# Kernel tuning notes

Measured on AMD Instinct MI355X. Metric: run time of the kernel, lower is better.

Reference implementation:

```python
import jax, jax.numpy as jnp
import numpy as np

N = 100000   # nodes
E = 600000   # edges
D = 128      # hidden_dim
R = 8        # edge_vocab_size (num_relations)
B = 64       # graphs in batch
V = 5000     # node_vocab_size
L = 3        # num_layers


def setup_inputs() -> dict:
    key = jax.random.key(0)
    ks = jax.random.split(key, 16)
    s = 1.0 / np.sqrt(D)
    node_type = jax.random.randint(ks[0], (N,), 0, V, dtype=jnp.int32)
    edge_index = jax.random.randint(ks[1], (2, E), 0, N, dtype=jnp.int32)
    edge_type = jax.random.randint(ks[2], (E,), 0, R, dtype=jnp.int32)
    batch = jnp.sort(jax.random.randint(ks[3], (N,), 0, B, dtype=jnp.int32))
    node_emb = jax.random.normal(ks[4], (V, D), dtype=jnp.float32)
    rel_w = jax.random.normal(ks[5], (L, R, D, D), dtype=jnp.float32) * s
    root_w = jax.random.normal(ks[6], (L, D, D), dtype=jnp.float32) * s
    bias = jnp.zeros((L, D), dtype=jnp.float32)
    risk_w1 = jax.random.normal(ks[7], (D, D), dtype=jnp.float32) * s
    risk_b1 = jnp.zeros((D,), dtype=jnp.float32)
    risk_w2 = jax.random.normal(ks[8], (D, 1), dtype=jnp.float32) * s
    risk_b2 = jnp.zeros((1,), dtype=jnp.float32)
    safe_w1 = jax.random.normal(ks[9], (D, D), dtype=jnp.float32) * s
    safe_b1 = jnp.zeros((D,), dtype=jnp.float32)
    safe_w2 = jax.random.normal(ks[10], (D, 1), dtype=jnp.float32) * s
    safe_b2 = jnp.zeros((1,), dtype=jnp.float32)
    return dict(node_type=node_type, edge_index=edge_index, edge_type=edge_type,
                batch=batch, node_emb=node_emb, rel_w=rel_w, root_w=root_w,
                bias=bias, risk_w1=risk_w1, risk_b1=risk_b1, risk_w2=risk_w2,
                risk_b2=risk_b2, safe_w1=safe_w1, safe_b1=safe_b1,
                safe_w2=safe_w2, safe_b2=safe_b2)


def _rgcn_layer(x, edge_index, edge_type, Wrel, Wroot, b):
    # PyG RGCNConv: per-relation mean aggregation of source features,
    # then relation-specific linear + root transform + bias.
    src, dst = edge_index[0], edge_index[1]
    seg = dst * R + edge_type                      # combined (node, relation) id
    msgs = x[src]                                  # [E, D] gather
    sums = jax.ops.segment_sum(msgs, seg, num_segments=N * R)      # [N*R, D]
    cnt = jax.ops.segment_sum(jnp.ones((E,), x.dtype), seg, num_segments=N * R)
    mean = sums / jnp.maximum(cnt, 1.0)[:, None]
    mean = mean.reshape(N, R, D)
    out = jnp.einsum('nrd,rde->ne', mean, Wrel) + x @ Wroot + b
    return out


def _mlp_head(g, w1, b1, w2, b2):
    h = jax.nn.relu(g @ w1 + b1)
    return (h @ w2 + b2).squeeze(-1)               # dropout is identity in eval


def reference(node_type, edge_index, edge_type, batch, node_emb, rel_w, root_w,
              bias, risk_w1, risk_b1, risk_w2, risk_b2, safe_w1, safe_b1,
              safe_w2, safe_b2):
    x = node_emb[node_type]                        # [N, D]
    for l in range(L):                             # fixed small layer loop
        x = jax.nn.relu(_rgcn_layer(x, edge_index, edge_type,
                                    rel_w[l], root_w[l], bias[l]))
    # global_mean_pool over graph ids
    g_sum = jax.ops.segment_sum(x, batch, num_segments=B)          # [B, D]
    g_cnt = jax.ops.segment_sum(jnp.ones((N,), x.dtype), batch, num_segments=B)
    g = g_sum / jnp.maximum(g_cnt, 1.0)[:, None]
    risk_pred = _mlp_head(g, risk_w1, risk_b1, risk_w2, risk_b2)   # [B]
    safe_logit = _mlp_head(g, safe_w1, safe_b1, safe_w2, safe_b2)  # [B]
    return risk_pred, safe_logit
```

## Files before the change

kernel.cpp:

```cpp
#include <hip/hip_runtime.h>
#include <hip/hip_bf16.h>

#define N_NODES 100000
#define N_EDGES 600000
#define DIM     128
#define N_REL   8
#define N_GRAPH 64
#define N_LAYER 3
#define NR      (N_NODES * N_REL)
#define NB1     782

typedef __attribute__((ext_vector_type(4))) float float4v;
typedef __attribute__((ext_vector_type(2))) float float2v;
typedef unsigned long long ull;

__device__ __forceinline__ int gswz8(int row, int g) {
    return row * 16 + (g ^ (row & 15));
}

__global__ void k_hist(const int* __restrict__ ei, const int* __restrict__ et,
                       int* __restrict__ counts) {
    int e = blockIdx.x * 256 + threadIdx.x;
    if (e < N_EDGES) {
        int seg = ei[N_EDGES + e] * N_REL + et[e];
        atomicAdd(&counts[seg], 1);
    }
}

__global__ __launch_bounds__(256) void k_scan1(const int* __restrict__ cnts,
                                               int* __restrict__ part,
                                               int* __restrict__ bsum) {
    __shared__ int sh[256];
    int t = threadIdx.x;
    int base = blockIdx.x * 1024 + t * 4;
    int v0 = (base + 0 < NR) ? cnts[base + 0] : 0;
    int v1 = (base + 1 < NR) ? cnts[base + 1] : 0;
    int v2 = (base + 2 < NR) ? cnts[base + 2] : 0;
    int v3 = (base + 3 < NR) ? cnts[base + 3] : 0;
    int tot = v0 + v1 + v2 + v3;
    sh[t] = tot;
    __syncthreads();
    for (int off = 1; off < 256; off <<= 1) {
        int x = (t >= off) ? sh[t - off] : 0;
        __syncthreads();
        sh[t] += x;
        __syncthreads();
    }
    int exc = sh[t] - tot;
    if (base + 0 < NR) part[base + 0] = exc;
    if (base + 1 < NR) part[base + 1] = exc + v0;
    if (base + 2 < NR) part[base + 2] = exc + v0 + v1;
    if (base + 3 < NR) part[base + 3] = exc + v0 + v1 + v2;
    if (t == 255) bsum[blockIdx.x] = sh[t];
}

__global__ __launch_bounds__(1024) void k_scan2(int* __restrict__ bsum, int nb) {
    __shared__ int sh[1024];
    int t = threadIdx.x;
    int v = (t < nb) ? bsum[t] : 0;
    sh[t] = v;
    __syncthreads();
    for (int off = 1; off < 1024; off <<= 1) {
        int x = (t >= off) ? sh[t - off] : 0;
        __syncthreads();
        sh[t] += x;
        __syncthreads();
    }
    if (t < nb) bsum[t] = sh[t] - v;
}

__global__ void k_scan3(const int* __restrict__ part, const int* __restrict__ bsum,
                        int* __restrict__ rowptr, int* __restrict__ cursor) {
    int i = blockIdx.x * 256 + threadIdx.x;
    if (i < NR) {
        int v = part[i] + bsum[i >> 10];
        rowptr[i] = v;
        cursor[i] = v;
    }
    if (i == 0) rowptr[NR] = N_EDGES;
}

__global__ void k_scatter(const int* __restrict__ ei, const int* __restrict__ et,
                          int* __restrict__ cursor, int* __restrict__ srcs) {
    int e = blockIdx.x * 256 + threadIdx.x;
    if (e < N_EDGES) {
        int seg = ei[N_EDGES + e] * N_REL + et[e];
        int p = atomicAdd(&cursor[seg], 1);
        srcs[p] = ei[e];
    }
}

__global__ void k_gather8(const int* __restrict__ nt, const float* __restrict__ emb,
                          unsigned int* __restrict__ x8) {
    int gid = blockIdx.x * 256 + threadIdx.x;
    if (gid < N_NODES * 32) {
        int n = gid >> 5, up = gid & 31;
        const float* row = emb + (size_t)nt[n] * DIM;
        int p0 = up * 4;
        float f0 = row[((p0 + 0) & 7) * 16 + ((p0 + 0) >> 3)];
        float f1 = row[((p0 + 1) & 7) * 16 + ((p0 + 1) >> 3)];
        float f2 = row[((p0 + 2) & 7) * 16 + ((p0 + 2) >> 3)];
        float f3 = row[((p0 + 3) & 7) * 16 + ((p0 + 3) >> 3)];
        int u = __builtin_amdgcn_cvt_pk_fp8_f32(f0, f1, 0, false);
        u = __builtin_amdgcn_cvt_pk_fp8_f32(f2, f3, u, true);
        x8[gid] = (unsigned int)u;
    }
}

#define W8_TOTAL (N_LAYER * 9 * 8192)
__global__ void k_wprep9(const float* __restrict__ relw, const float* __restrict__ rootw,
                         unsigned short* __restrict__ W8) {
    int gid = blockIdx.x * 256 + threadIdx.x;
    if (gid < W8_TOTAL) {
        int l = gid / (9 * 8192);
        int rem = gid - l * 9 * 8192;
        int r = rem >> 13;
        int idx = rem & 8191;
        int n = idx >> 6, p2 = idx & 63;
        int pos0 = 2 * p2, pos1 = 2 * p2 + 1;
        int k0 = (pos0 & 7) * 16 + (pos0 >> 3);
        int k1 = (pos1 & 7) * 16 + (pos1 >> 3);
        float w0, w1;
        if (r < 8) {
            const float* base = relw + ((size_t)(l * 8 + r) * 128) * 128 + n;
            w0 = base[(size_t)k0 * 128];
            w1 = base[(size_t)k1 * 128];
        } else {
            const float* base = rootw + (size_t)l * 128 * 128 + n;
            w0 = base[(size_t)k0 * 128];
            w1 = base[(size_t)k1 * 128];
        }
        int pk = __builtin_amdgcn_cvt_pk_fp8_f32(w0, w1, 0, false);
        W8[gid] = (unsigned short)(pk & 0xffff);
    }
}

__global__ __launch_bounds__(256) void k_agg(
    const unsigned int* __restrict__ x8,
    const int* __restrict__ rowptr,
    const int* __restrict__ srcs,
    unsigned int* __restrict__ Ag8,
    int d0, int rows, int srows)
{
    const int t = threadIdx.x;
    const int wv = t >> 6, lane = t & 63;
    const int q = lane >> 4, j = lane & 15;
    const int nb0 = (blockIdx.x * 4 + wv) * 4;
    if (nb0 >= rows) return;
    const int myn = nb0 + q;
    const bool nvalid = (myn < rows);

    int pr = 0;
    {
        int idx = (d0 + nb0) * 8 + lane;
        if (idx > NR) idx = NR;
        if (lane < 33) pr = rowptr[idx];
    }
    const int P0 = __shfl(pr, 0);
    const int Dtot = __shfl(pr, 32) - P0;

    int my_src = 0;
    if (lane < Dtot) my_src = srcs[P0 + lane];

    const uint2* x2p = (const uint2*)x8;
    uint2* Agf = (uint2*)Ag8;

    for (int r = 0; r < 8; ++r) {
        int e0 = __shfl(pr, q * 8 + r);
        int e1 = __shfl(pr, q * 8 + r + 1);
        int cnt = e1 - e0;
        int m1 = max(cnt, __shfl_xor(cnt, 16));
        int maxc = max(m1, __shfl_xor(m1, 32));
        float2v A0 = {0.f, 0.f}, A1 = {0.f, 0.f}, A2 = {0.f, 0.f}, A3 = {0.f, 0.f};
        int k = 0;
        for (; k + 2 <= maxc; k += 2) {
            int ei0 = e0 + k, ei1 = e0 + k + 1;
            int r0 = ei0 - P0, r1 = ei1 - P0;
            int s0 = __shfl(my_src, r0 & 63);
            int s1 = __shfl(my_src, r1 & 63);
            if (r0 >= 64) s0 = srcs[ei0];
            if (r1 >= 64) s1 = srcs[ei1];
            bool v0 = (k < cnt), v1 = (k + 1 < cnt);
            uint2 u0, u1;
            if (v0) u0 = x2p[(size_t)s0 * 16 + j];
            if (v1) u1 = x2p[(size_t)s1 * 16 + j];
            if (v0) {
                A0 += __builtin_amdgcn_cvt_pk_f32_fp8((int)u0.x, false);
                A1 += __builtin_amdgcn_cvt_pk_f32_fp8((int)u0.x, true);
                A2 += __builtin_amdgcn_cvt_pk_f32_fp8((int)u0.y, false);
                A3 += __builtin_amdgcn_cvt_pk_f32_fp8((int)u0.y, true);
            }
            if (v1) {
                A0 += __builtin_amdgcn_cvt_pk_f32_fp8((int)u1.x, false);
                A1 += __builtin_amdgcn_cvt_pk_f32_fp8((int)u1.x, true);
                A2 += __builtin_amdgcn_cvt_pk_f32_fp8((int)u1.y, false);
                A3 += __builtin_amdgcn_cvt_pk_f32_fp8((int)u1.y, true);
            }
        }
        if (k < maxc) {
            int ei = e0 + k;
            int ridx = ei - P0;
            int s = __shfl(my_src, ridx & 63);
            if (ridx >= 64) s = srcs[ei];
            if (k < cnt) {
                uint2 u = x2p[(size_t)s * 16 + j];
                A0 += __builtin_amdgcn_cvt_pk_f32_fp8((int)u.x, false);
                A1 += __builtin_amdgcn_cvt_pk_f32_fp8((int)u.x, true);
                A2 += __builtin_amdgcn_cvt_pk_f32_fp8((int)u.y, false);
                A3 += __builtin_amdgcn_cvt_pk_f32_fp8((int)u.y, true);
            }
        }
        float inv = (cnt > 0) ? 1.0f / (float)cnt : 0.f;
        float2v iv = {inv, inv};
        A0 *= iv; A1 *= iv; A2 *= iv; A3 *= iv;
        int u0 = __builtin_amdgcn_cvt_pk_fp8_f32(A0.x, A0.y, 0, false);
        u0 = __builtin_amdgcn_cvt_pk_fp8_f32(A1.x, A1.y, u0, true);
        int u1 = __builtin_amdgcn_cvt_pk_fp8_f32(A2.x, A2.y, 0, false);
        u1 = __builtin_amdgcn_cvt_pk_fp8_f32(A3.x, A3.y, u1, true);
        if (nvalid) {
            uint2 v; v.x = (unsigned int)u0; v.y = (unsigned int)u1;
            Agf[(size_t)r * srows * 16 + (size_t)(myn >> 4) * 256 + j * 16 + (myn & 15)] = v;
        }
    }
}

#define BM2 128
__global__ __launch_bounds__(256) void k_gemm(
    const unsigned int* __restrict__ Ag8,
    const unsigned int* __restrict__ x8in,
    unsigned int* __restrict__ x8out,
    const unsigned short* __restrict__ W8,
    const float* __restrict__ bias,
    int d0, int srows)
{
    __shared__ __align__(16) ull Bls[4096];
    const int t = threadIdx.x;
    const int wv = t >> 6, lane = t & 63;
    const int quad = lane >> 4, l15 = lane & 15;
    const int m0 = d0 + blockIdx.x * BM2;

    float4v acc[2][8];
#pragma unroll
    for (int nt = 0; nt < 8; ++nt) {
        float bc = bias[nt * 16 + l15];
        acc[0][nt] = (float4v){bc, bc, bc, bc};
        acc[1][nt] = (float4v){bc, bc, bc, bc};
    }

    const size_t pstride = (size_t)srows * 16;
    const ull* Ag = (const ull*)Ag8 + ((size_t)((m0 - d0) >> 4) + 2 * wv) * 256;
    const ull* Xr = (const ull*)x8in;

    ull aC[8], aN[8], bR[8];
    {
        const ull* Wc = (const ull*)W8;
#pragma unroll
        for (int i = 0; i < 8; ++i) {
            aC[i] = Ag[(size_t)(i >> 2) * 256 + (i & 3) * 64 + lane];
            bR[i] = Wc[t + 256 * i];
        }
    }
#pragma unroll
    for (int i = 0; i < 8; ++i) {
        int idx = t + 256 * i;
        Bls[gswz8(idx >> 4, idx & 15)] = bR[i];
    }
    __syncthreads();

    for (int c = 0; c < 9; ++c) {
        const int cur = (c & 1) * 2048;
        if (c < 8) {
            if (c + 1 < 8) {
                const ull* Ac = Ag + (size_t)(c + 1) * pstride;
#pragma unroll
                for (int i = 0; i < 8; ++i)
                    aN[i] = Ac[(size_t)(i >> 2) * 256 + (i & 3) * 64 + lane];
            } else {
#pragma unroll
                for (int i = 0; i < 8; ++i) {
                    int rt = i >> 2, kk = i & 3;
                    aN[i] = Xr[(size_t)(m0 + wv * 32 + rt * 16 + l15) * 16 + kk * 4 + quad];
                }
            }
            const ull* Wc = (const ull*)(W8 + (size_t)(c + 1) * 8192);
#pragma unroll
            for (int i = 0; i < 8; ++i) bR[i] = Wc[t + 256 * i];
        }
#pragma unroll
        for (int kk = 0; kk < 4; ++kk) {
            long long a0 = (long long)aC[kk];
            long long a1 = (long long)aC[4 + kk];
            int g = kk * 4 + quad;
#pragma unroll
            for (int nt = 0; nt < 8; ++nt) {
                long long b8 = (long long)Bls[cur + (nt * 16 + l15) * 16 + (g ^ l15)];
                acc[0][nt] = __builtin_amdgcn_mfma_f32_16x16x32_fp8_fp8(a0, b8, acc[0][nt], 0, 0, 0);
                acc[1][nt] = __builtin_amdgcn_mfma_f32_16x16x32_fp8_fp8(a1, b8, acc[1][nt], 0, 0, 0);
            }
        }
        if (c < 8) {
            const int nxt = ((c + 1) & 1) * 2048;
#pragma unroll
            for (int i = 0; i < 8; ++i) {
                int idx = t + 256 * i;
                Bls[nxt + gswz8(idx >> 4, idx & 15)] = bR[i];
                aC[i] = aN[i];
            }
            __syncthreads();
        }
    }
    ull* outs = (ull*)x8out;
#pragma unroll
    for (int rt = 0; rt < 2; ++rt) {
#pragma unroll
        for (int i = 0; i < 4; ++i) {
            int row = m0 + wv * 32 + rt * 16 + quad * 4 + i;
            float v0 = acc[rt][0][i], v1 = acc[rt][1][i];
            float v2 = acc[rt][2][i], v3 = acc[rt][3][i];
            float v4 = acc[rt][4][i], v5 = acc[rt][5][i];
            float v6 = acc[rt][6][i], v7 = acc[rt][7][i];
            v0 = v0 > 0.f ? v0 : 0.f;  v1 = v1 > 0.f ? v1 : 0.f;
            v2 = v2 > 0.f ? v2 : 0.f;  v3 = v3 > 0.f ? v3 : 0.f;
            v4 = v4 > 0.f ? v4 : 0.f;  v5 = v5 > 0.f ? v5 : 0.f;
            v6 = v6 > 0.f ? v6 : 0.f;  v7 = v7 > 0.f ? v7 : 0.f;
            int lo = __builtin_amdgcn_cvt_pk_fp8_f32(v0, v1, 0, false);
            lo = __builtin_amdgcn_cvt_pk_fp8_f32(v2, v3, lo, true);
            int hi = __builtin_amdgcn_cvt_pk_fp8_f32(v4, v5, 0, false);
            hi = __builtin_amdgcn_cvt_pk_fp8_f32(v6, v7, hi, true);
            if (row < N_NODES) {
                ull w = ((ull)(unsigned int)hi << 32) | (unsigned int)lo;
                outs[(size_t)row * 16 + l15] = w;
            }
        }
    }
}

__global__ __launch_bounds__(256) void k_pool(const unsigned int* __restrict__ x8,
                                              const int* __restrict__ batch,
                                              float* __restrict__ gsum,
                                              int* __restrict__ gcnt) {
    const int wv = threadIdx.x >> 6, lane = threadIdx.x & 63;
    const int n0 = (blockIdx.x * 4 + wv) * 64;
    if (n0 >= N_NODES) return;
    int n1 = n0 + 64;
    if (n1 > N_NODES) n1 = N_NODES;
    const int nb = n1 - n0;
    const unsigned short* xs = (const unsigned short*)x8;
    int bb = batch[n0 + (lane < nb ? lane : nb - 1)];
    float2v A = {0.f, 0.f};
    int run = 0;
    int cur = __shfl(bb, 0);
    for (int base = 0; base < nb; base += 8) {
        unsigned int u[8];
        int m = nb - base;
#pragma unroll
        for (int qq = 0; qq < 8; ++qq)
            if (qq < m) u[qq] = xs[(size_t)(n0 + base + qq) * 64 + lane];
#pragma unroll
        for (int qq = 0; qq < 8; ++qq) {
            if (qq < m) {
                int b = __shfl(bb, base + qq);
                if (b != cur) {
                    atomicAdd(&gsum[cur * 128 + lane * 2], A.x);
                    atomicAdd(&gsum[cur * 128 + lane * 2 + 1], A.y);
                    if (lane == 0) atomicAdd(&gcnt[cur], run);
                    A = (float2v){0.f, 0.f};
                    run = 0;
                    cur = b;
                }
                A += __builtin_amdgcn_cvt_pk_f32_fp8((int)u[qq], false);
                ++run;
            }
        }
    }
    atomicAdd(&gsum[cur * 128 + lane * 2], A.x);
    atomicAdd(&gsum[cur * 128 + lane * 2 + 1], A.y);
    if (lane == 0) atomicAdd(&gcnt[cur], run);
}

__global__ __launch_bounds__(128) void k_heads(
    const float* __restrict__ gsum, const int* __restrict__ gcnt,
    const float* __restrict__ rw1, const float* __restrict__ rb1,
    const float* __restrict__ rw2, const float* __restrict__ rb2,
    const float* __restrict__ sw1, const float* __restrict__ sb1,
    const float* __restrict__ sw2, const float* __restrict__ sb2,
    float* __restrict__ out) {
    __shared__ float g[128];
    __shared__ float parts[2];
    int b = blockIdx.x, t = threadIdx.x;
    int c = gcnt[b];
    float invc = 1.0f / (float)(c > 0 ? c : 1);
    g[((t & 7) << 4) | (t >> 3)] = gsum[b * 128 + t] * invc;
    __syncthreads();
    float acc = rb1[t];
    for (int d = 0; d < 128; ++d) acc += g[d] * rw1[d * 128 + t];
    float h = acc > 0.f ? acc : 0.f;
    float p = h * rw2[t];
    for (int o = 32; o > 0; o >>= 1) p += __shfl_down(p, o);
    if ((t & 63) == 0) parts[t >> 6] = p;
    __syncthreads();
    if (t == 0) out[b] = parts[0] + parts[1] + rb2[0];
    __syncthreads();
    acc = sb1[t];
    for (int d = 0; d < 128; ++d) acc += g[d] * sw1[d * 128 + t];
    h = acc > 0.f ? acc : 0.f;
    p = h * sw2[t];
    for (int o = 32; o > 0; o >>= 1) p += __shfl_down(p, o);
    if ((t & 63) == 0) parts[t >> 6] = p;
    __syncthreads();
    if (t == 0) out[64 + b] = parts[0] + parts[1] + sb2[0];
}

extern "C" void kernel_launch(void* const* d_in, const int* in_sizes, int n_in,
                              void* d_out, int out_size, void* d_ws, size_t ws_size,
                              hipStream_t stream) {
    const int*   node_type  = (const int*)d_in[0];
    const int*   edge_index = (const int*)d_in[1];
    const int*   edge_type  = (const int*)d_in[2];
    const int*   batch      = (const int*)d_in[3];
    const float* node_emb   = (const float*)d_in[4];
    const float* rel_w      = (const float*)d_in[5];
    const float* root_w     = (const float*)d_in[6];
    const float* bias       = (const float*)d_in[7];
    const float* rw1        = (const float*)d_in[8];
    const float* rb1        = (const float*)d_in[9];
    const float* rw2        = (const float*)d_in[10];
    const float* rb2        = (const float*)d_in[11];
    const float* sw1        = (const float*)d_in[12];
    const float* sb1        = (const float*)d_in[13];
    const float* sw2        = (const float*)d_in[14];
    const float* sb2        = (const float*)d_in[15];
    float* out = (float*)d_out;

    char* ws = (char*)d_ws;
    size_t off = 0;
    auto alloc = [&](size_t bytes) -> void* {
        void* p = ws + off;
        off += (bytes + 255) & ~(size_t)255;
        return p;
    };
    unsigned int*   x8a    = (unsigned int*)alloc((size_t)N_NODES * 32 * 4);
    unsigned int*   x8b    = (unsigned int*)alloc((size_t)N_NODES * 32 * 4);
    int*            rowptr = (int*)alloc((size_t)(NR + 1) * 4);
    int*            srcs   = (int*)alloc((size_t)N_EDGES * 4);
    int*            bsum   = (int*)alloc(1024 * 4);
    unsigned short* W8     = (unsigned short*)alloc((size_t)W8_TOTAL * 2);
    float*          gsum   = (float*)alloc((64 * 128 + 64) * 4);
    int*            gcnt   = (int*)(gsum + 64 * 128);
    size_t off_common = off;
    int*            cursor = (int*)alloc((size_t)NR * 4);
    int*            counts = (int*)alloc((size_t)NR * 4);
    size_t off_sort = off;
    if (off_sort > ws_size) return;
    unsigned int*   Ag8    = (unsigned int*)(ws + off_common);
    size_t avail = ws_size - off_common;
    long max_rows = (avail > 32768) ? (long)((avail - 32768) / 1024) : 0;
    int srows = (int)((max_rows / 64) * 64);
    if (srows > N_NODES + 63) srows = ((N_NODES + 63) / 64) * 64;
    if (srows < 128) return;

    hipMemsetAsync(counts, 0, (size_t)NR * 4, stream);
    hipMemsetAsync(gsum, 0, (size_t)(64 * 128 + 64) * 4, stream);
    k_hist<<<(N_EDGES + 255) / 256, 256, 0, stream>>>(edge_index, edge_type, counts);
    k_scan1<<<NB1, 256, 0, stream>>>(counts, cursor, bsum);
    k_scan2<<<1, 1024, 0, stream>>>(bsum, NB1);
    k_scan3<<<(NR + 255) / 256, 256, 0, stream>>>(cursor, bsum, rowptr, cursor);
    k_scatter<<<(N_EDGES + 255) / 256, 256, 0, stream>>>(edge_index, edge_type, cursor, srcs);

    k_gather8<<<(N_NODES * 32 + 255) / 256, 256, 0, stream>>>(node_type, node_emb, x8a);
    k_wprep9<<<(W8_TOTAL + 255) / 256, 256, 0, stream>>>(rel_w, root_w, W8);

    unsigned int* xcur = x8a;
    unsigned int* xnext = x8b;
    for (int l = 0; l < N_LAYER; ++l) {
        const unsigned short* W8l = W8 + (size_t)l * 9 * 8192;
        const float* bl = bias + (size_t)l * 128;
        for (int d0 = 0; d0 < N_NODES; d0 += srows) {
            int rows = N_NODES - d0;
            if (rows > srows) rows = srows;
            int ab = (rows + 15) / 16;
            int gb = (rows + BM2 - 1) / BM2;
            k_agg<<<ab, 256, 0, stream>>>(xcur, rowptr, srcs, Ag8, d0, rows, srows);
            k_gemm<<<gb, 256, 0, stream>>>(Ag8, xcur, xnext, W8l, bl, d0, srows);
        }
        unsigned int* tmp = xcur; xcur = xnext; xnext = tmp;
    }

    k_pool<<<(N_NODES + 255) / 256, 256, 0, stream>>>(xcur, batch, gsum, gcnt);
    k_heads<<<64, 128, 0, stream>>>(gsum, gcnt, rw1, rb1, rw2, rb2,
                                    sw1, sb1, sw2, sb2, out);
}
```

Measured before the change: 421.9 us.

## Merge prep kernels and fuse mean pooling into last-layer GEMM epilogue

Combines the histogram, embedding gather, weight prep and graph-count kernels into one block-partitioned prep launch to cut launch overhead. The final layer's GEMM no longer writes fp8 node features; it accumulates ReLU outputs straight into per-graph sums, first through LDS slots and then global atomics, which removes the separate pool kernel and one fp8 round-trip. The pooled sums now stay in fp32 rather than going through fp8 quantisation, and the chunk size is rounded to 128 rows. The cost is heavy LDS and global atomic traffic in the last GEMM epilogue.

```diff
diff --git a/kernel.cpp b/kernel.cpp
--- a/kernel.cpp
+++ b/kernel.cpp
@@ -18,82 +18,29 @@
     return row * 16 + (g ^ (row & 15));
 }
 
-__global__ void k_hist(const int* __restrict__ ei, const int* __restrict__ et,
-                       int* __restrict__ counts) {
-    int e = blockIdx.x * 256 + threadIdx.x;
-    if (e < N_EDGES) {
-        int seg = ei[N_EDGES + e] * N_REL + et[e];
-        atomicAdd(&counts[seg], 1);
-    }
-}
-
-__global__ __launch_bounds__(256) void k_scan1(const int* __restrict__ cnts,
-                                               int* __restrict__ part,
-                                               int* __restrict__ bsum) {
-    __shared__ int sh[256];
-    int t = threadIdx.x;
-    int base = blockIdx.x * 1024 + t * 4;
-    int v0 = (base + 0 < NR) ? cnts[base + 0] : 0;
-    int v1 = (base + 1 < NR) ? cnts[base + 1] : 0;
-    int v2 = (base + 2 < NR) ? cnts[base + 2] : 0;
-    int v3 = (base + 3 < NR) ? cnts[base + 3] : 0;
-    int tot = v0 + v1 + v2 + v3;
-    sh[t] = tot;
-    __syncthreads();
-    for (int off = 1; off < 256; off <<= 1) {
-        int x = (t >= off) ? sh[t - off] : 0;
-        __syncthreads();
-        sh[t] += x;
-        __syncthreads();
-    }
-    int exc = sh[t] - tot;
-    if (base + 0 < NR) part[base + 0] = exc;
-    if (base + 1 < NR) part[base + 1] = exc + v0;
-    if (base + 2 < NR) part[base + 2] = exc + v0 + v1;
-    if (base + 3 < NR) part[base + 3] = exc + v0 + v1 + v2;
-    if (t == 255) bsum[blockIdx.x] = sh[t];
-}
-
-__global__ __launch_bounds__(1024) void k_scan2(int* __restrict__ bsum, int nb) {
-    __shared__ int sh[1024];
-    int t = threadIdx.x;
-    int v = (t < nb) ? bsum[t] : 0;
-    sh[t] = v;
-    __syncthreads();
-    for (int off = 1; off < 1024; off <<= 1) {
-        int x = (t >= off) ? sh[t - off] : 0;
-        __syncthreads();
-        sh[t] += x;
-        __syncthreads();
-    }
-    if (t < nb) bsum[t] = sh[t] - v;
-}
-
-__global__ void k_scan3(const int* __restrict__ part, const int* __restrict__ bsum,
-                        int* __restrict__ rowptr, int* __restrict__ cursor) {
-    int i = blockIdx.x * 256 + threadIdx.x;
-    if (i < NR) {
-        int v = part[i] + bsum[i >> 10];
-        rowptr[i] = v;
-        cursor[i] = v;
-    }
-    if (i == 0) rowptr[NR] = N_EDGES;
-}
-
-__global__ void k_scatter(const int* __restrict__ ei, const int* __restrict__ et,
-                          int* __restrict__ cursor, int* __restrict__ srcs) {
-    int e = blockIdx.x * 256 + threadIdx.x;
-    if (e < N_EDGES) {
-        int seg = ei[N_EDGES + e] * N_REL + et[e];
-        int p = atomicAdd(&cursor[seg], 1);
-        srcs[p] = ei[e];
-    }
-}
-
-__global__ void k_gather8(const int* __restrict__ nt, const float* __restrict__ emb,
-                          unsigned int* __restrict__ x8) {
-    int gid = blockIdx.x * 256 + threadIdx.x;
-    if (gid < N_NODES * 32) {
+#define W8_TOTAL (N_LAYER * 9 * 8192)
+#define PB_HIST  2344
+#define PB_GATH  12500
+#define PB_WPRE  864
+#define PB_BCNT  391
+#define PB_TOTAL (PB_HIST + PB_GATH + PB_WPRE + PB_BCNT)
+
+__global__ __launch_bounds__(256) void k_prep(
+    const int* __restrict__ ei, const int* __restrict__ et, int* __restrict__ counts,
+    const int* __restrict__ nt, const float* __restrict__ emb, unsigned int* __restrict__ x8,
+    const float* __restrict__ relw, const float* __restrict__ rootw,
+    unsigned short* __restrict__ W8,
+    const int* __restrict__ batch, int* __restrict__ gcnt)
+{
+    const int b = blockIdx.x, t = threadIdx.x;
+    if (b < PB_HIST) {
+        int e = b * 256 + t;
+        if (e < N_EDGES) {
+            int seg = ei[N_EDGES + e] * N_REL + et[e];
+            atomicAdd(&counts[seg], 1);
+        }
+    } else if (b < PB_HIST + PB_GATH) {
+        int gid = (b - PB_HIST) * 256 + t;
         int n = gid >> 5, up = gid & 31;
         const float* row = emb + (size_t)nt[n] * DIM;
         int p0 = up * 4;
@@ -104,14 +51,8 @@
         int u = __builtin_amdgcn_cvt_pk_fp8_f32(f0, f1, 0, false);
         u = __builtin_amdgcn_cvt_pk_fp8_f32(f2, f3, u, true);
         x8[gid] = (unsigned int)u;
-    }
-}
-
-#define W8_TOTAL (N_LAYER * 9 * 8192)
-__global__ void k_wprep9(const float* __restrict__ relw, const float* __restrict__ rootw,
-                         unsigned short* __restrict__ W8) {
-    int gid = blockIdx.x * 256 + threadIdx.x;
-    if (gid < W8_TOTAL) {
+    } else if (b < PB_HIST + PB_GATH + PB_WPRE) {
+        int gid = (b - PB_HIST - PB_GATH) * 256 + t;
         int l = gid / (9 * 8192);
         int rem = gid - l * 9 * 8192;
         int r = rem >> 13;
@@ -132,6 +73,72 @@
         }
         int pk = __builtin_amdgcn_cvt_pk_fp8_f32(w0, w1, 0, false);
         W8[gid] = (unsigned short)(pk & 0xffff);
+    } else {
+        int i = (b - PB_HIST - PB_GATH - PB_WPRE) * 256 + t;
+        if (i < N_NODES) atomicAdd(&gcnt[batch[i]], 1);
+    }
+}
+
+__global__ __launch_bounds__(256) void k_scan1(const int* __restrict__ cnts,
+                                               int* __restrict__ part,
+                                               int* __restrict__ bsum) {
+    __shared__ int sh[256];
+    int t = threadIdx.x;
+    int base = blockIdx.x * 1024 + t * 4;
+    int v0 = (base + 0 < NR) ? cnts[base + 0] : 0;
+    int v1 = (base + 1 < NR) ? cnts[base + 1] : 0;
+    int v2 = (base + 2 < NR) ? cnts[base + 2] : 0;
+    int v3 = (base + 3 < NR) ? cnts[base + 3] : 0;
+    int tot = v0 + v1 + v2 + v3;
+    sh[t] = tot;
+    __syncthreads();
+    for (int off = 1; off < 256; off <<= 1) {
+        int x = (t >= off) ? sh[t - off] : 0;
+        __syncthreads();
+        sh[t] += x;
+        __syncthreads();
+    }
+    int exc = sh[t] - tot;
+    if (base + 0 < NR) part[base + 0] = exc;
+    if (base + 1 < NR) part[base + 1] = exc + v0;
+    if (base + 2 < NR) part[base + 2] = exc + v0 + v1;
+    if (base + 3 < NR) part[base + 3] = exc + v0 + v1 + v2;
+    if (t == 255) bsum[blockIdx.x] = sh[t];
+}
+
+__global__ __launch_bounds__(1024) void k_scan2(int* __restrict__ bsum, int nb) {
+    __shared__ int sh[1024];
+    int t = threadIdx.x;
+    int v = (t < nb) ? bsum[t] : 0;
+    sh[t] = v;
+    __syncthreads();
+    for (int off = 1; off < 1024; off <<= 1) {
+        int x = (t >= off) ? sh[t - off] : 0;
+        __syncthreads();
+        sh[t] += x;
+        __syncthreads();
+    }
+    if (t < nb) bsum[t] = sh[t] - v;
+}
+
+__global__ void k_scan3(const int* __restrict__ part, const int* __restrict__ bsum,
+                        int* __restrict__ rowptr, int* __restrict__ cursor) {
+    int i = blockIdx.x * 256 + threadIdx.x;
+    if (i < NR) {
+        int v = part[i] + bsum[i >> 10];
+        rowptr[i] = v;
+        cursor[i] = v;
+    }
+    if (i == 0) rowptr[NR] = N_EDGES;
+}
+
+__global__ void k_scatter(const int* __restrict__ ei, const int* __restrict__ et,
+                          int* __restrict__ cursor, int* __restrict__ srcs) {
+    int e = blockIdx.x * 256 + threadIdx.x;
+    if (e < N_EDGES) {
+        int seg = ei[N_EDGES + e] * N_REL + et[e];
+        int p = atomicAdd(&cursor[seg], 1);
+        srcs[p] = ei[e];
     }
 }
 
@@ -231,7 +238,9 @@
     unsigned int* __restrict__ x8out,
     const unsigned short* __restrict__ W8,
     const float* __restrict__ bias,
-    int d0, int srows)
+    const int* __restrict__ batch,
+    float* __restrict__ gsum,
+    int d0, int srows, int last)
 {
     __shared__ __align__(16) ull Bls[4096];
     const int t = threadIdx.x;
@@ -309,73 +318,62 @@
             __syncthreads();
         }
     }
-    ull* outs = (ull*)x8out;
-#pragma unroll
-    for (int rt = 0; rt < 2; ++rt) {
-#pragma unroll
-        for (int i = 0; i < 4; ++i) {
-            int row = m0 + wv * 32 + rt * 16 + quad * 4 + i;
-            float v0 = acc[rt][0][i], v1 = acc[rt][1][i];
-            float v2 = acc[rt][2][i], v3 = acc[rt][3][i];
-            float v4 = acc[rt][4][i], v5 = acc[rt][5][i];
-            float v6 = acc[rt][6][i], v7 = acc[rt][7][i];
-            v0 = v0 > 0.f ? v0 : 0.f;  v1 = v1 > 0.f ? v1 : 0.f;
-            v2 = v2 > 0.f ? v2 : 0.f;  v3 = v3 > 0.f ? v3 : 0.f;
-            v4 = v4 > 0.f ? v4 : 0.f;  v5 = v5 > 0.f ? v5 : 0.f;
-            v6 = v6 > 0.f ? v6 : 0.f;  v7 = v7 > 0.f ? v7 : 0.f;
-            int lo = __builtin_amdgcn_cvt_pk_fp8_f32(v0, v1, 0, false);
-            lo = __builtin_amdgcn_cvt_pk_fp8_f32(v2, v3, lo, true);
-            int hi = __builtin_amdgcn_cvt_pk_fp8_f32(v4, v5, 0, false);
-            hi = __builtin_amdgcn_cvt_pk_fp8_f32(v6, v7, hi, true);
-            if (row < N_NODES) {
-                ull w = ((ull)(unsigned int)hi << 32) | (unsigned int)lo;
-                outs[(size_t)row * 16 + l15] = w;
-            }
-        }
-    }
-}
-
-__global__ __launch_bounds__(256) void k_pool(const unsigned int* __restrict__ x8,
-                                              const int* __restrict__ batch,
-                                              float* __restrict__ gsum,
-                                              int* __restrict__ gcnt) {
-    const int wv = threadIdx.x >> 6, lane = threadIdx.x & 63;
-    const int n0 = (blockIdx.x * 4 + wv) * 64;
-    if (n0 >= N_NODES) return;
-    int n1 = n0 + 64;
-    if (n1 > N_NODES) n1 = N_NODES;
-    const int nb = n1 - n0;
-    const unsigned short* xs = (const unsigned short*)x8;
-    int bb = batch[n0 + (lane < nb ? lane : nb - 1)];
-    float2v A = {0.f, 0.f};
-    int run = 0;
-    int cur = __shfl(bb, 0);
-    for (int base = 0; base < nb; base += 8) {
-        unsigned int u[8];
-        int m = nb - base;
-#pragma unroll
-        for (int qq = 0; qq < 8; ++qq)
-            if (qq < m) u[qq] = xs[(size_t)(n0 + base + qq) * 64 + lane];
-#pragma unroll
-        for (int qq = 0; qq < 8; ++qq) {
-            if (qq < m) {
-                int b = __shfl(bb, base + qq);
-                if (b != cur) {
-                    atomicAdd(&gsum[cur * 128 + lane * 2], A.x);
-                    atomicAdd(&gsum[cur * 128 + lane * 2 + 1], A.y);
-                    if (lane == 0) atomicAdd(&gcnt[cur], run);
-                    A = (float2v){0.f, 0.f};
-                    run = 0;
-                    cur = b;
+    if (!last) {
+        ull* outs = (ull*)x8out;
+#pragma unroll
+        for (int rt = 0; rt < 2; ++rt) {
+#pragma unroll
+            for (int i = 0; i < 4; ++i) {
+                int row = m0 + wv * 32 + rt * 16 + quad * 4 + i;
+                float v0 = acc[rt][0][i], v1 = acc[rt][1][i];
+                float v2 = acc[rt][2][i], v3 = acc[rt][3][i];
+                float v4 = acc[rt][4][i], v5 = acc[rt][5][i];
+                float v6 = acc[rt][6][i], v7 = acc[rt][7][i];
+                v0 = v0 > 0.f ? v0 : 0.f;  v1 = v1 > 0.f ? v1 : 0.f;
+                v2 = v2 > 0.f ? v2 : 0.f;  v3 = v3 > 0.f ? v3 : 0.f;
+                v4 = v4 > 0.f ? v4 : 0.f;  v5 = v5 > 0.f ? v5 : 0.f;
+                v6 = v6 > 0.f ? v6 : 0.f;  v7 = v7 > 0.f ? v7 : 0.f;
+                int lo = __builtin_amdgcn_cvt_pk_fp8_f32(v0, v1, 0, false);
+                lo = __builtin_amdgcn_cvt_pk_fp8_f32(v2, v3, lo, true);
+                int hi = __builtin_amdgcn_cvt_pk_fp8_f32(v4, v5, 0, false);
+                hi = __builtin_amdgcn_cvt_pk_fp8_f32(v6, v7, hi, true);
+                if (row < N_NODES) {
+                    ull w = ((ull)(unsigned int)hi << 32) | (unsigned int)lo;
+                    outs[(size_t)row * 16 + l15] = w;
                 }
-                A += __builtin_amdgcn_cvt_pk_f32_fp8((int)u[qq], false);
-                ++run;
-            }
-        }
-    }
-    atomicAdd(&gsum[cur * 128 + lane * 2], A.x);
-    atomicAdd(&gsum[cur * 128 + lane * 2 + 1], A.y);
-    if (lane == 0) atomicAdd(&gcnt[cur], run);
+            }
+        }
+    } else {
+        __syncthreads();
+        float* plds = (float*)Bls;
+        for (int i = t; i < 8 * 128; i += 256) plds[i] = 0.f;
+        const int bmin = batch[m0];
+        __syncthreads();
+#pragma unroll
+        for (int rt = 0; rt < 2; ++rt) {
+#pragma unroll
+            for (int i = 0; i < 4; ++i) {
+                int row = m0 + wv * 32 + rt * 16 + quad * 4 + i;
+                if (row < N_NODES) {
+                    int slot = batch[row] - bmin;
+#pragma unroll
+                    for (int nt = 0; nt < 8; ++nt) {
+                        float v = acc[rt][nt][i];
+                        v = v > 0.f ? v : 0.f;
+                        int col = nt * 16 + l15;
+                        if (slot < 8) atomicAdd(&plds[slot * 128 + col], v);
+                        else atomicAdd(&gsum[(size_t)(bmin + slot) * 128 + col], v);
+                    }
+                }
+            }
+        }
+        __syncthreads();
+        for (int i = t; i < 8 * 128; i += 256) {
+            float v = plds[i];
+            int gb = bmin + (i >> 7);
+            if (v != 0.f && gb < N_GRAPH) atomicAdd(&gsum[gb * 128 + (i & 127)], v);
+        }
+    }
 }
 
 __global__ __launch_bounds__(128) void k_heads(
@@ -390,7 +388,7 @@
     int b = blockIdx.x, t = threadIdx.x;
     int c = gcnt[b];
     float invc = 1.0f / (float)(c > 0 ? c : 1);
-    g[((t & 7) << 4) | (t >> 3)] = gsum[b * 128 + t] * invc;
+    g[t] = gsum[b * 128 + t] * invc;
     __syncthreads();
     float acc = rb1[t];
     for (int d = 0; d < 128; ++d) acc += g[d] * rw1[d * 128 + t];
@@ -455,38 +453,38 @@
     unsigned int*   Ag8    = (unsigned int*)(ws + off_common);
     size_t avail = ws_size - off_common;
     long max_rows = (avail > 32768) ? (long)((avail - 32768) / 1024) : 0;
-    int srows = (int)((max_rows / 64) * 64);
-    if (srows > N_NODES + 63) srows = ((N_NODES + 63) / 64) * 64;
+    int srows = (int)((max_rows / 128) * 128);
+    if (srows > N_NODES + 127) srows = ((N_NODES + 127) / 128) * 128;
     if (srows < 128) return;
 
     hipMemsetAsync(counts, 0, (size_t)NR * 4, stream);
     hipMemsetAsync(gsum, 0, (size_t)(64 * 128 + 64) * 4, stream);
-    k_hist<<<(N_EDGES + 255) / 256, 256, 0, stream>>>(edge_index, edge_type, counts);
+    k_prep<<<PB_TOTAL, 256, 0, stream>>>(edge_index, edge_type, counts,
+                                         node_type, node_emb, x8a,
+                                         rel_w, root_w, W8, batch, gcnt);
     k_scan1<<<NB1, 256, 0, stream>>>(counts, cursor, bsum);
     k_scan2<<<1, 1024, 0, stream>>>(bsum, NB1);
     k_scan3<<<(NR + 255) / 256, 256, 0, stream>>>(cursor, bsum, rowptr, cursor);
     k_scatter<<<(N_EDGES + 255) / 256, 256, 0, stream>>>(edge_index, edge_type, cursor, srcs);
-
-    k_gather8<<<(N_NODES * 32 + 255) / 256, 256, 0, stream>>>(node_type, node_emb, x8a);
-    k_wprep9<<<(W8_TOTAL + 255) / 256, 256, 0, stream>>>(rel_w, root_w, W8);
 
     unsigned int* xcur = x8a;
     unsigned int* xnext = x8b;
     for (int l = 0; l < N_LAYER; ++l) {
         const unsigned short* W8l = W8 + (size_t)l * 9 * 8192;
         const float* bl = bias + (size_t)l * 128;
+        const int last = (l == N_LAYER - 1) ? 1 : 0;
         for (int d0 = 0; d0 < N_NODES; d0 += srows) {
             int rows = N_NODES - d0;
             if (rows > srows) rows = srows;
             int ab = (rows + 15) / 16;
             int gb = (rows + BM2 - 1) / BM2;
             k_agg<<<ab, 256, 0, stream>>>(xcur, rowptr, srcs, Ag8, d0, rows, srows);
-            k_gemm<<<gb, 256, 0, stream>>>(Ag8, xcur, xnext, W8l, bl, d0, srows);
+            k_gemm<<<gb, 256, 0, stream>>>(Ag8, xcur, xnext, W8l, bl,
+                                           batch, gsum, d0, srows, last);
         }
         unsigned int* tmp = xcur; xcur = xnext; xnext = tmp;
     }
 
-    k_pool<<<(N_NODES + 255) / 256, 256, 0, stream>>>(xcur, batch, gsum, gcnt);
     k_heads<<<64, 128, 0, stream>>>(gsum, gcnt, rw1, rb1, rw2, rb2,
                                     sw1, sb1, sw2, sb2, out);
 }
```

Result: slower. 989.2 us (+134.4%).
